# Kernel optimization log

Measured on AMD Instinct MI355X. Metric: run time of the kernel, lower is better.

The kernel has to match this reference:

```python
import jax, jax.numpy as jnp
import numpy as np

NEG = -9e15

def setup_inputs() -> dict:
    key = jax.random.key(0)
    k1, k2, k3, k4, k5 = jax.random.split(key, 5)
    N, Fin, Fout = 8192, 256, 128
    h = jax.random.normal(k1, (N, Fin), dtype=jnp.float32)
    adj = jax.random.randint(k2, (N, N), 0, 2, dtype=jnp.int32)
    # Parameters (xavier_uniform with gain=1.414 for a1/a2; kaiming-like for W is fine as random init)
    lim_w = float(np.sqrt(6.0 / (Fin + Fout)))
    W = jax.random.uniform(k3, (Fout, Fin), dtype=jnp.float32, minval=-lim_w, maxval=lim_w)
    lim_a = float(1.414 * np.sqrt(6.0 / (Fout + 1)))
    a1 = jax.random.uniform(k4, (Fout, 1), dtype=jnp.float32, minval=-lim_a, maxval=lim_a)
    a2 = jax.random.uniform(k5, (Fout, 1), dtype=jnp.float32, minval=-lim_a, maxval=lim_a)
    return {"h": h, "adj": adj, "W": W, "a1": a1, "a2": a2}

def reference(h, adj, W, a1, a2):
    Wh = h @ W.T                                   # [N, Fout]
    s1 = (Wh @ a1)                                 # [N, 1]
    s2 = (Wh @ a2)                                 # [N, 1]
    e = jax.nn.leaky_relu(s1 + s2.T, 0.2)          # [N, N]
    att = jnp.where(adj > 0, e, jnp.float32(NEG))
    att = jax.nn.softmax(att, axis=1)
    h_prime = att @ Wh                             # [N, Fout]
    return jax.nn.elu(h_prime)
```

## Files before the change

### kernel.cpp

```cpp
#include <hip/hip_runtime.h>
#include <cstdint>
#include <cstddef>

#define N_NODES 8192
#define FIN 256
#define FOUT 128
#define MT 32
#define KC 256
#define JS 4
#define JW (N_NODES / JS)
#define NCHS (JW / KC)
#define LOG2E 1.4426950408889634f

typedef __attribute__((ext_vector_type(8))) short bf16x8;
typedef __attribute__((ext_vector_type(4))) float f32x4;
typedef __attribute__((ext_vector_type(2))) unsigned int u32x2;

__device__ __forceinline__ float bf2f(unsigned short u) {
    union { unsigned int i; float f; } v; v.i = ((unsigned int)u) << 16; return v.f;
}
__device__ __forceinline__ unsigned short f2bf(float f) {
    union { float f; unsigned int i; } v; v.f = f;
    unsigned int r = (v.i + 0x7FFFu + ((v.i >> 16) & 1u)) >> 16;
    return (unsigned short)r;
}
__device__ __forceinline__ unsigned int pack_bf16(float a, float b) {
    return (unsigned)f2bf(a) | ((unsigned)f2bf(b) << 16);
}

__device__ __forceinline__ size_t whb_idx(int j, int f) {
    return ((size_t)((j >> 5) * 8 + (f >> 4)) << 9) + (((j >> 3) & 3) << 7)
         + ((f & 15) << 3) + (j & 7);
}

__global__ __launch_bounds__(256) void pack_kernel(const int* __restrict__ adj,
                                                   unsigned long long* __restrict__ bits) {
    const int t = threadIdx.x;
    const int lane = t & 63;
    const int wv = t >> 6;
    const int wid = blockIdx.x * 4 + wv;
#pragma unroll
    for (int pass = 0; pass < 2; ++pass) {
        const int row = wid + pass * 4096;
        const int* ar = adj + (size_t)row * N_NODES;
        unsigned long long k0 = 0, k1 = 0;
#pragma unroll
        for (int seg = 0; seg < 64; ++seg) {
            unsigned long long m = __ballot(ar[seg * 64 + lane] > 0);
            if (lane == seg) k0 = m;
        }
#pragma unroll
        for (int seg = 0; seg < 64; ++seg) {
            unsigned long long m = __ballot(ar[4096 + seg * 64 + lane] > 0);
            if (lane == seg) k1 = m;
        }
        unsigned long long* br = bits + (size_t)row * 128;
        br[lane] = k0;
        br[64 + lane] = k1;
    }
}

__global__ __launch_bounds__(256) void wh_kernel(const float* __restrict__ h,
                                                 const float* __restrict__ W,
                                                 unsigned short* __restrict__ whB) {
    __shared__ float hT[64][FIN + 5];
    const int t = threadIdx.x;
    const int i0 = blockIdx.x * 64;
    const int f0 = blockIdx.y * 32;
#pragma unroll
    for (int c = 0; c < 16; ++c) {
        int chunk = c * 256 + t;
        int row = chunk >> 6, col = (chunk & 63) * 4;
        f32x4 v = *(const f32x4*)&h[(size_t)(i0 + row) * FIN + col];
        hT[row][col] = v[0]; hT[row][col + 1] = v[1];
        hT[row][col + 2] = v[2]; hT[row][col + 3] = v[3];
    }
    __syncthreads();
    const int lane = t & 63;
    const int fb8 = __builtin_amdgcn_readfirstlane(f0 + (t >> 6) * 8);
    const float* w0 = W + (size_t)fb8 * FIN;
    float acc[8] = {0.f, 0.f, 0.f, 0.f, 0.f, 0.f, 0.f, 0.f};
    for (int k = 0; k < FIN; k += 4) {
        float h0 = hT[lane][k],     h1 = hT[lane][k + 1];
        float h2 = hT[lane][k + 2], h3 = hT[lane][k + 3];
#pragma unroll
        for (int c = 0; c < 8; ++c) {
            const float* wr = w0 + c * FIN;
            acc[c] += h0 * wr[k] + h1 * wr[k + 1] + h2 * wr[k + 2] + h3 * wr[k + 3];
        }
    }
    const int i = i0 + lane;
#pragma unroll
    for (int c = 0; c < 8; ++c)
        whB[whb_idx(i, fb8 + c)] = f2bf(acc[c]);
}

__global__ __launch_bounds__(256) void s_kernel(const unsigned short* __restrict__ whB,
                                                const float* __restrict__ a1,
                                                const float* __restrict__ a2,
                                                float* __restrict__ s1,
                                                float* __restrict__ s2) {
    __shared__ float p1[4][64], p2[4][64];
    const int t = threadIdx.x;
    const int l = t & 63;
    const int g = t >> 6;
    const int i = blockIdx.x * 64 + l;
    float acc1 = 0.f, acc2 = 0.f;
#pragma unroll
    for (int fb = g * 2; fb < g * 2 + 2; ++fb) {
#pragma unroll
        for (int sl = 0; sl < 16; ++sl) {
            int f = fb * 16 + sl;
            float v = bf2f(whB[whb_idx(i, f)]);
            acc1 += v * a1[f];
            acc2 += v * a2[f];
        }
    }
    p1[g][l] = acc1; p2[g][l] = acc2;
    __syncthreads();
    if (g == 0) {
        s1[i] = (p1[0][l] + p1[1][l] + p1[2][l] + p1[3][l]) * LOG2E;
        s2[i] = (p2[0][l] + p2[1][l] + p2[2][l] + p2[3][l]) * LOG2E;
    }
}

__global__ __launch_bounds__(256) void gat_kernel(const unsigned long long* __restrict__ bits,
                                                  const unsigned short* __restrict__ whB,
                                                  const float* __restrict__ s1,
                                                  const float* __restrict__ s2,
                                                  float* __restrict__ out,
                                                  float* __restrict__ nums,
                                                  float* __restrict__ dens) {
    __shared__ __align__(16) unsigned short sP[MT][KC + 8];
    __shared__ float sDen[MT];
    __shared__ float sS1[MT];
    const int t = threadIdx.x;
    const int slice = blockIdx.x & (JS - 1);
    const int i0 = (blockIdx.x >> 2) * MT;
    const int jb = slice * JW;
    const int kb0 = slice * (JW / 32);
    float* __restrict__ num = slice ? (nums + (size_t)(slice - 1) * N_NODES * FOUT) : out;
    float* __restrict__ den = dens + (size_t)slice * N_NODES;
    if (t < MT) { sDen[t] = 0.f; sS1[t] = s1[i0 + t]; }
    __syncthreads();

    const int r0 = t >> 4;
    const int s  = t & 15;
    const int lane = t & 63;
    const int quad = lane >> 4;
    const int sl = lane & 15;
    const int wv = t >> 6;
    const unsigned long long* bRow0 = bits + (size_t)(i0 + r0) * 128;
    const unsigned long long* bRow1 = bRow0 + (size_t)16 * 128;
    const int shft = (s & 3) * 16;
    const float s1a = sS1[r0];
    const float s1b = sS1[r0 + 16];

    f32x4 acc00 = {0.f,0.f,0.f,0.f}, acc01 = {0.f,0.f,0.f,0.f};
    f32x4 acc10 = {0.f,0.f,0.f,0.f}, acc11 = {0.f,0.f,0.f,0.f};

    int w0i = (jb >> 6) + (s >> 2);
    unsigned long long bw0 = bRow0[w0i];
    unsigned long long bw1 = bRow1[w0i];
    f32x4 sv[4];
#pragma unroll
    for (int q = 0; q < 4; ++q) sv[q] = *(const f32x4*)&s2[jb + s * 16 + q * 4];

    for (int ch = 0; ch < NCHS; ++ch) {
        unsigned int m0 = (unsigned int)(bw0 >> shft) & 0xFFFFu;
        unsigned int m1 = (unsigned int)(bw1 >> shft) & 0xFFFFu;
        float part0 = 0.f, part1 = 0.f;
#pragma unroll
        for (int q = 0; q < 4; ++q) {
            float p0[4], p1v[4];
#pragma unroll
            for (int r = 0; r < 4; ++r) {
                float y0 = s1a + sv[q][r];
                float y1 = s1b + sv[q][r];
                y0 = fmaxf(y0, 0.2f * y0);
                y1 = fmaxf(y1, 0.2f * y1);
                float e0 = __builtin_amdgcn_exp2f(y0);
                float e1 = __builtin_amdgcn_exp2f(y1);
                int b = q * 4 + r;
                p0[r]  = ((m0 >> b) & 1u) ? e0 : 0.f;
                p1v[r] = ((m1 >> b) & 1u) ? e1 : 0.f;
                part0 += p0[r];
                part1 += p1v[r];
            }
            u32x2 pk0, pk1;
            pk0.x = pack_bf16(p0[0], p0[1]);   pk0.y = pack_bf16(p0[2], p0[3]);
            pk1.x = pack_bf16(p1v[0], p1v[1]); pk1.y = pack_bf16(p1v[2], p1v[3]);
            *(u32x2*)&sP[r0][s * 16 + q * 4] = pk0;
            *(u32x2*)&sP[r0 + 16][s * 16 + q * 4] = pk1;
        }
        if (ch + 1 < NCHS) {
            int jn = jb + (ch + 1) * KC;
            int wni = (jn >> 6) + (s >> 2);
            bw0 = bRow0[wni];
            bw1 = bRow1[wni];
#pragma unroll
            for (int q = 0; q < 4; ++q) sv[q] = *(const f32x4*)&s2[jn + s * 16 + q * 4];
        }
        part0 += __shfl_xor(part0, 1); part1 += __shfl_xor(part1, 1);
        part0 += __shfl_xor(part0, 2); part1 += __shfl_xor(part1, 2);
        part0 += __shfl_xor(part0, 4); part1 += __shfl_xor(part1, 4);
        part0 += __shfl_xor(part0, 8); part1 += __shfl_xor(part1, 8);
        if (s == 0) { sDen[r0] += part0; sDen[r0 + 16] += part1; }
        __syncthreads();
#pragma unroll
        for (int kq = 0; kq < KC / 32; ++kq) {
            bf16x8 a0  = *(const bf16x8*)&sP[sl][kq * 32 + quad * 8];
            bf16x8 a1f = *(const bf16x8*)&sP[16 + sl][kq * 32 + quad * 8];
            int kb = kb0 + ch * (KC / 32) + kq;
            const unsigned short* t0 = whB + ((size_t)(kb * 8 + wv * 2) << 9) + lane * 8;
            bf16x8 b0 = *(const bf16x8*)t0;
            bf16x8 b1 = *(const bf16x8*)(t0 + 512);
            acc00 = __builtin_amdgcn_mfma_f32_16x16x32_bf16(a0,  b0, acc00, 0, 0, 0);
            acc01 = __builtin_amdgcn_mfma_f32_16x16x32_bf16(a0,  b1, acc01, 0, 0, 0);
            acc10 = __builtin_amdgcn_mfma_f32_16x16x32_bf16(a1f, b0, acc10, 0, 0, 0);
            acc11 = __builtin_amdgcn_mfma_f32_16x16x32_bf16(a1f, b1, acc11, 0, 0, 0);
        }
        __syncthreads();
    }
    if (t < MT) den[i0 + t] = sDen[t];
#pragma unroll
    for (int m = 0; m < 2; ++m) {
#pragma unroll
        for (int nn = 0; nn < 2; ++nn) {
            f32x4 a = (m == 0) ? (nn == 0 ? acc00 : acc01) : (nn == 0 ? acc10 : acc11);
#pragma unroll
            for (int r = 0; r < 4; ++r) {
                int row = m * 16 + quad * 4 + r;
                num[(size_t)(i0 + row) * FOUT + wv * 32 + nn * 16 + sl] = a[r];
            }
        }
    }
}

__global__ __launch_bounds__(256) void fin_kernel(float* __restrict__ out,
                                                  const float* __restrict__ nums,
                                                  const float* __restrict__ dens) {
    const int idx = blockIdx.x * 256 + threadIdx.x;
    const int i = idx >> 7;
    const size_t NF = (size_t)N_NODES * FOUT;
    float numv = out[idx] + nums[idx] + nums[NF + idx] + nums[2 * NF + idx];
    float denv = dens[i] + dens[N_NODES + i] + dens[2 * N_NODES + i] + dens[3 * N_NODES + i];
    float v = numv / fmaxf(denv, 1e-30f);
    out[idx] = (v > 0.f) ? v : expm1f(v);
}

extern "C" void kernel_launch(void* const* d_in, const int* in_sizes, int n_in,
                              void* d_out, int out_size, void* d_ws, size_t ws_size,
                              hipStream_t stream) {
    const float* h   = (const float*)d_in[0];
    const int*   adj = (const int*)d_in[1];
    const float* W   = (const float*)d_in[2];
    const float* a1  = (const float*)d_in[3];
    const float* a2  = (const float*)d_in[4];

    char* ws = (char*)d_ws;
    unsigned short*     whB  = (unsigned short*)ws;
    unsigned long long* bits = (unsigned long long*)(ws + (2u << 20));
    float* s1   = (float*)(ws + (10u << 20));
    float* s2   = s1 + N_NODES;
    float* dens = s2 + N_NODES;
    float* nums = dens + 4 * N_NODES;
    float* out  = (float*)d_out;

    pack_kernel<<<dim3(1024), 256, 0, stream>>>(adj, bits);
    wh_kernel<<<dim3(N_NODES / 64, FOUT / 32), 256, 0, stream>>>(h, W, whB);
    s_kernel<<<dim3(N_NODES / 64), 256, 0, stream>>>(whB, a1, a2, s1, s2);
    gat_kernel<<<dim3((N_NODES / MT) * JS), 256, 0, stream>>>(bits, whB, s1, s2,
                                                              out, nums, dens);
    fin_kernel<<<dim3(N_NODES * FOUT / 256), 256, 0, stream>>>(out, nums, dens);
}
```

Before: 433.5 us.

## Fuse adjacency bit-packing into attention kernel by reading int adj directly

Removes the separate pack_kernel that compressed the int32 adjacency matrix into bitmasks. The attention kernel now reads int32 adjacency values straight from global memory per chunk and tests them inline. It also writes the bf16 probability tile to shared memory as wider 16-byte stores. This saves one kernel launch and one write-then-read of the bitmask, but each gat block now reads 32x more adjacency bytes and no longer prefetches the next chunk's inputs.

```diff
diff --git a/kernel.cpp b/kernel.cpp
--- a/kernel.cpp
+++ b/kernel.cpp
@@ -14,7 +14,8 @@
 
 typedef __attribute__((ext_vector_type(8))) short bf16x8;
 typedef __attribute__((ext_vector_type(4))) float f32x4;
-typedef __attribute__((ext_vector_type(2))) unsigned int u32x2;
+typedef __attribute__((ext_vector_type(4))) int i32x4;
+typedef __attribute__((ext_vector_type(4))) unsigned int u32x4;
 
 __device__ __forceinline__ float bf2f(unsigned short u) {
     union { unsigned int i; float f; } v; v.i = ((unsigned int)u) << 16; return v.f;
@@ -31,33 +32,6 @@
 __device__ __forceinline__ size_t whb_idx(int j, int f) {
     return ((size_t)((j >> 5) * 8 + (f >> 4)) << 9) + (((j >> 3) & 3) << 7)
          + ((f & 15) << 3) + (j & 7);
-}
-
-__global__ __launch_bounds__(256) void pack_kernel(const int* __restrict__ adj,
-                                                   unsigned long long* __restrict__ bits) {
-    const int t = threadIdx.x;
-    const int lane = t & 63;
-    const int wv = t >> 6;
-    const int wid = blockIdx.x * 4 + wv;
-#pragma unroll
-    for (int pass = 0; pass < 2; ++pass) {
-        const int row = wid + pass * 4096;
-        const int* ar = adj + (size_t)row * N_NODES;
-        unsigned long long k0 = 0, k1 = 0;
-#pragma unroll
-        for (int seg = 0; seg < 64; ++seg) {
-            unsigned long long m = __ballot(ar[seg * 64 + lane] > 0);
-            if (lane == seg) k0 = m;
-        }
-#pragma unroll
-        for (int seg = 0; seg < 64; ++seg) {
-            unsigned long long m = __ballot(ar[4096 + seg * 64 + lane] > 0);
-            if (lane == seg) k1 = m;
-        }
-        unsigned long long* br = bits + (size_t)row * 128;
-        br[lane] = k0;
-        br[64 + lane] = k1;
-    }
 }
 
 __global__ __launch_bounds__(256) void wh_kernel(const float* __restrict__ h,
@@ -124,7 +98,7 @@
     }
 }
 
-__global__ __launch_bounds__(256) void gat_kernel(const unsigned long long* __restrict__ bits,
+__global__ __launch_bounds__(256) void gat_kernel(const int* __restrict__ adj,
                                                   const unsigned short* __restrict__ whB,
                                                   const float* __restrict__ s1,
                                                   const float* __restrict__ s2,
@@ -150,26 +124,26 @@
     const int quad = lane >> 4;
     const int sl = lane & 15;
     const int wv = t >> 6;
-    const unsigned long long* bRow0 = bits + (size_t)(i0 + r0) * 128;
-    const unsigned long long* bRow1 = bRow0 + (size_t)16 * 128;
-    const int shft = (s & 3) * 16;
+    const int* __restrict__ aRow0 = adj + (size_t)(i0 + r0) * N_NODES + jb;
+    const int* __restrict__ aRow1 = aRow0 + (size_t)16 * N_NODES;
     const float s1a = sS1[r0];
     const float s1b = sS1[r0 + 16];
 
     f32x4 acc00 = {0.f,0.f,0.f,0.f}, acc01 = {0.f,0.f,0.f,0.f};
     f32x4 acc10 = {0.f,0.f,0.f,0.f}, acc11 = {0.f,0.f,0.f,0.f};
 
-    int w0i = (jb >> 6) + (s >> 2);
-    unsigned long long bw0 = bRow0[w0i];
-    unsigned long long bw1 = bRow1[w0i];
-    f32x4 sv[4];
-#pragma unroll
-    for (int q = 0; q < 4; ++q) sv[q] = *(const f32x4*)&s2[jb + s * 16 + q * 4];
-
     for (int ch = 0; ch < NCHS; ++ch) {
-        unsigned int m0 = (unsigned int)(bw0 >> shft) & 0xFFFFu;
-        unsigned int m1 = (unsigned int)(bw1 >> shft) & 0xFFFFu;
+        const int cb = ch * KC + s * 16;
+        i32x4 av0[4], av1[4];
+        f32x4 sv[4];
+#pragma unroll
+        for (int q = 0; q < 4; ++q) {
+            av0[q] = *(const i32x4*)&aRow0[cb + q * 4];
+            av1[q] = *(const i32x4*)&aRow1[cb + q * 4];
+            sv[q]  = *(const f32x4*)&s2[jb + cb + q * 4];
+        }
         float part0 = 0.f, part1 = 0.f;
+        unsigned int w0[8], w1[8];
 #pragma unroll
         for (int q = 0; q < 4; ++q) {
             float p0[4], p1v[4];
@@ -181,26 +155,24 @@
                 y1 = fmaxf(y1, 0.2f * y1);
                 float e0 = __builtin_amdgcn_exp2f(y0);
                 float e1 = __builtin_amdgcn_exp2f(y1);
-                int b = q * 4 + r;
-                p0[r]  = ((m0 >> b) & 1u) ? e0 : 0.f;
-                p1v[r] = ((m1 >> b) & 1u) ? e1 : 0.f;
+                p0[r]  = (av0[q][r] > 0) ? e0 : 0.f;
+                p1v[r] = (av1[q][r] > 0) ? e1 : 0.f;
                 part0 += p0[r];
                 part1 += p1v[r];
             }
-            u32x2 pk0, pk1;
-            pk0.x = pack_bf16(p0[0], p0[1]);   pk0.y = pack_bf16(p0[2], p0[3]);
-            pk1.x = pack_bf16(p1v[0], p1v[1]); pk1.y = pack_bf16(p1v[2], p1v[3]);
-            *(u32x2*)&sP[r0][s * 16 + q * 4] = pk0;
-            *(u32x2*)&sP[r0 + 16][s * 16 + q * 4] = pk1;
-        }
-        if (ch + 1 < NCHS) {
-            int jn = jb + (ch + 1) * KC;
-            int wni = (jn >> 6) + (s >> 2);
-            bw0 = bRow0[wni];
-            bw1 = bRow1[wni];
-#pragma unroll
-            for (int q = 0; q < 4; ++q) sv[q] = *(const f32x4*)&s2[jn + s * 16 + q * 4];
-        }
+            w0[2 * q]     = pack_bf16(p0[0], p0[1]);
+            w0[2 * q + 1] = pack_bf16(p0[2], p0[3]);
+            w1[2 * q]     = pack_bf16(p1v[0], p1v[1]);
+            w1[2 * q + 1] = pack_bf16(p1v[2], p1v[3]);
+        }
+        u32x4 ra = {w0[0], w0[1], w0[2], w0[3]};
+        u32x4 rb = {w0[4], w0[5], w0[6], w0[7]};
+        u32x4 rc = {w1[0], w1[1], w1[2], w1[3]};
+        u32x4 rd = {w1[4], w1[5], w1[6], w1[7]};
+        *(u32x4*)&sP[r0][s * 16]          = ra;
+        *(u32x4*)&sP[r0][s * 16 + 8]      = rb;
+        *(u32x4*)&sP[r0 + 16][s * 16]     = rc;
+        *(u32x4*)&sP[r0 + 16][s * 16 + 8] = rd;
         part0 += __shfl_xor(part0, 1); part1 += __shfl_xor(part1, 1);
         part0 += __shfl_xor(part0, 2); part1 += __shfl_xor(part1, 2);
         part0 += __shfl_xor(part0, 4); part1 += __shfl_xor(part1, 4);
@@ -259,18 +231,16 @@
     const float* a2  = (const float*)d_in[4];
 
     char* ws = (char*)d_ws;
-    unsigned short*     whB  = (unsigned short*)ws;
-    unsigned long long* bits = (unsigned long long*)(ws + (2u << 20));
-    float* s1   = (float*)(ws + (10u << 20));
+    unsigned short* whB = (unsigned short*)ws;
+    float* s1   = (float*)(ws + (4u << 20));
     float* s2   = s1 + N_NODES;
     float* dens = s2 + N_NODES;
     float* nums = dens + 4 * N_NODES;
     float* out  = (float*)d_out;
 
-    pack_kernel<<<dim3(1024), 256, 0, stream>>>(adj, bits);
     wh_kernel<<<dim3(N_NODES / 64, FOUT / 32), 256, 0, stream>>>(h, W, whB);
     s_kernel<<<dim3(N_NODES / 64), 256, 0, stream>>>(whB, a1, a2, s1, s2);
-    gat_kernel<<<dim3((N_NODES / MT) * JS), 256, 0, stream>>>(bits, whB, s1, s2,
+    gat_kernel<<<dim3((N_NODES / MT) * JS), 256, 0, stream>>>(adj, whB, s1, s2,
                                                               out, nums, dens);
     fin_kernel<<<dim3(N_NODES * FOUT / 256), 256, 0, stream>>>(out, nums, dens);
 }
```

After: 406.7 us. 6.2% less time.
